# Performance work log

Hardware: AMD Instinct MI355X
Metric: run time of the kernel (lower is better)

Reference implementation:

```python
import jax, jax.numpy as jnp
import numpy as np

B, S, D, H = 2, 2048, 1024, 16
DH = D // H
DFF = 4 * D
EPS = 1e-5
NEG = -1e9


def _layernorm(x, gamma, beta):
    mu = jnp.mean(x, axis=-1, keepdims=True)
    var = jnp.mean(jnp.square(x - mu), axis=-1, keepdims=True)
    return (x - mu) * jax.lax.rsqrt(var + EPS) * gamma + beta


def setup_inputs() -> dict:
    key = jax.random.key(0)
    ks = jax.random.split(key, 12)
    s = 0.02
    X = jax.random.normal(ks[0], (B, S, D), dtype=jnp.float32)
    # causal mask (True = attend)
    attention_mask = jnp.tril(jnp.ones((S, S), dtype=bool))
    return {
        "X": X,
        "attention_mask": attention_mask,
        "gamma1": jnp.ones((D,), jnp.float32),
        "beta1": jnp.zeros((D,), jnp.float32),
        "Wq": jax.random.normal(ks[1], (H, D, DH), jnp.float32) * s,
        "bq": jnp.zeros((H, DH), jnp.float32),
        "Wk": jax.random.normal(ks[2], (H, D, DH), jnp.float32) * s,
        "bk": jnp.zeros((H, DH), jnp.float32),
        "Wv": jax.random.normal(ks[3], (H, D, DH), jnp.float32) * s,
        "bv": jnp.zeros((H, DH), jnp.float32),
        "W0": jax.random.normal(ks[4], (D, D), jnp.float32) * s,
        "b0": jnp.zeros((D,), jnp.float32),
        "gamma2": jnp.ones((D,), jnp.float32),
        "beta2": jnp.zeros((D,), jnp.float32),
        "W1": jax.random.normal(ks[5], (D, DFF), jnp.float32) * s,
        "b1": jnp.zeros((DFF,), jnp.float32),
        "W2": jax.random.normal(ks[6], (DFF, D), jnp.float32) * s,
        "b2": jnp.zeros((D,), jnp.float32),
    }


def reference(X, attention_mask, gamma1, beta1, Wq, bq, Wk, bk, Wv, bv, W0, b0,
              gamma2, beta2, W1, b1, W2, b2):
    scale = 1.0 / np.sqrt(DH)
    # --- pre-LN MHA ---
    Xn = _layernorm(X, gamma1, beta1)
    # per-head projections, stacked: [B,H,S,DH]
    Q = jnp.einsum('bsd,hdk->bhsk', Xn, Wq) + bq[None, :, None, :]
    K = jnp.einsum('bsd,hdk->bhsk', Xn, Wk) + bk[None, :, None, :]
    V = jnp.einsum('bsd,hdk->bhsk', Xn, Wv) + bv[None, :, None, :]
    scores = jnp.einsum('bhsk,bhtk->bhst', Q, K) * scale
    scores = jnp.where(attention_mask, scores, NEG)
    weights = jax.nn.softmax(scores, axis=-1)
    attn = jnp.einsum('bhst,bhtv->bhsv', weights, V)  # [B,H,S,DH]
    # concat heads (head-major along feature dim, matching torch.cat order)
    attn = attn.transpose(0, 2, 1, 3).reshape(B, S, D)
    mha = attn @ W0 + b0
    X = mha + X  # residual (dropout = identity at eval)
    # --- pre-LN FFN ---
    Xn2 = _layernorm(X, gamma2, beta2)
    h = jax.nn.relu(Xn2 @ W1 + b1)
    ffn = h @ W2 + b2
    return ffn + X
```

## Files before the change

kernel.cpp:

```cpp
#include <hip/hip_runtime.h>
#include <hip/hip_bf16.h>

#define BB 2
#define SS 2048
#define DDIM 1024
#define HH 16
#define DHH 64
#define DFF_ 4096
#define BS 4096
#define NQKV 3072

typedef unsigned short u16;
using short8  = __attribute__((ext_vector_type(8))) short;
using floatx4 = __attribute__((ext_vector_type(4))) float;

__device__ __forceinline__ u16 f2b(float f){
  union { unsigned int u; float f; } v; v.f = f;
  unsigned int u = v.u;
  u += 0x7FFFu + ((u >> 16) & 1u);
  return (u16)(u >> 16);
}

__device__ __forceinline__ void gl2lds16(const u16* g, u16* l){
  __builtin_amdgcn_global_load_lds((const __attribute__((address_space(1))) void*)g,
                                   (__attribute__((address_space(3))) void*)l, 16, 0, 0);
}

__device__ __forceinline__ void ln_row(const float* __restrict__ x,
                                       const float* __restrict__ gamma,
                                       const float* __restrict__ beta,
                                       u16* __restrict__ y, int row, float* smem){
  const float4* xr = (const float4*)(x + (size_t)row * DDIM);
  int tid = threadIdx.x;
  float4 v = xr[tid];
  float s  = v.x + v.y + v.z + v.w;
  float ss = v.x*v.x + v.y*v.y + v.z*v.z + v.w*v.w;
  for (int o = 1; o < 64; o <<= 1){ s += __shfl_xor(s, o, 64); ss += __shfl_xor(ss, o, 64); }
  int wid = tid >> 6;
  if ((tid & 63) == 0){ smem[wid] = s; smem[wid + 4] = ss; }
  __syncthreads();
  s  = smem[0] + smem[1] + smem[2] + smem[3];
  ss = smem[4] + smem[5] + smem[6] + smem[7];
  float mu  = s / (float)DDIM;
  float var = ss / (float)DDIM - mu * mu;
  float rs  = rsqrtf(var + 1e-5f);
  const float4* gp = (const float4*)gamma;
  const float4* bp = (const float4*)beta;
  float4 g = gp[tid], b = bp[tid];
  u16* yr = y + (size_t)row * DDIM + tid*4;
  yr[0] = f2b((v.x - mu) * rs * g.x + b.x);
  yr[1] = f2b((v.y - mu) * rs * g.y + b.y);
  yr[2] = f2b((v.z - mu) * rs * g.z + b.z);
  yr[3] = f2b((v.w - mu) * rs * g.w + b.w);
}

__device__ __forceinline__ void tcast(const float* __restrict__ in, u16* __restrict__ out,
                                      int R, int C, int tile, float (*sh)[33]){
  int nr = R >> 5;
  int tr = tile % nr, tc = tile / nr;
  int r0 = tr * 32, c0 = tc * 32;
  int tx = threadIdx.x & 31, ty = threadIdx.x >> 5;
  for (int i = ty; i < 32; i += 8)
    sh[i][tx] = in[(size_t)(r0 + i) * C + c0 + tx];
  __syncthreads();
  for (int i = ty; i < 32; i += 8)
    out[(size_t)(c0 + i) * R + r0 + tx] = f2b(sh[tx][i]);
}

__global__ __launch_bounds__(256) void prep_ln1_k(
    const float* __restrict__ X, const float* __restrict__ g1, const float* __restrict__ be1,
    u16* __restrict__ Xn,
    const float* __restrict__ Wq, const float* __restrict__ Wk, const float* __restrict__ Wv,
    const float* __restrict__ W0, const float* __restrict__ W1,
    const float* __restrict__ bq, const float* __restrict__ bk, const float* __restrict__ bv,
    u16* __restrict__ wqkvT, u16* __restrict__ w0T, u16* __restrict__ w1T,
    float* __restrict__ biasQKV)
{
  __shared__ float sh[32][33];
  __shared__ float smem8[8];
  int id = blockIdx.x;
  if (id < 4096){
    ln_row(X, g1, be1, Xn, id, smem8);
  } else if (id < 7168){
    int lid2 = id - 4096;
    int which = lid2 >> 10, lid = lid2 & 1023;
    const float* src = which == 0 ? Wq : (which == 1 ? Wk : Wv);
    u16* dst = wqkvT + (size_t)which * 1048576;
    int bat = lid >> 6, t = lid & 63;
    tcast(src + (size_t)bat * 65536, dst + (size_t)bat * 65536, 1024, 64, t, sh);
  } else if (id < 8192){
    tcast(W0, w0T, 1024, 1024, id - 7168, sh);
  } else if (id < 12288){
    tcast(W1, w1T, 1024, 4096, id - 8192, sh);
  } else {
    int idx = (id - 12288) * 256 + threadIdx.x;
    if (idx < 3072){
      float v = idx < 1024 ? bq[idx] : (idx < 2048 ? bk[idx - 1024] : bv[idx - 2048]);
      biasQKV[idx] = v;
    }
  }
}

__global__ __launch_bounds__(256) void w2t_ln2_k(
    const float* __restrict__ X1, const float* __restrict__ g2, const float* __restrict__ be2,
    u16* __restrict__ Xn2, const float* __restrict__ W2, u16* __restrict__ w2T)
{
  __shared__ float sh[32][33];
  __shared__ float smem8[8];
  int id = blockIdx.x;
  if (id < 4096){
    ln_row(X1, g2, be2, Xn2, id, smem8);
  } else {
    int tile = id - 4096;
    int tr = tile / 32, tc = tile % 32;
    int r0 = tr * 32, c0 = tc * 32;
    int tx = threadIdx.x & 31, ty = threadIdx.x >> 5;
    for (int i = ty; i < 32; i += 8)
      sh[i][tx] = W2[(size_t)(r0 + i) * 1024 + c0 + tx];
    __syncthreads();
    for (int i = ty; i < 32; i += 8)
      w2T[(size_t)(c0 + i) * 4096 + r0 + tx] = f2b(sh[tx][i]);
  }
}

__global__ __launch_bounds__(256) void vt_k(const u16* __restrict__ QKV, u16* __restrict__ VT){
  __shared__ u16 t[32][33];
  int bh = blockIdx.z; int b = bh >> 4, h = bh & 15;
  int s0 = blockIdx.x * 32, d0 = blockIdx.y * 32;
  int tx = threadIdx.x & 31, ty = threadIdx.x >> 5;
  const u16* src = QKV + (size_t)b * SS * NQKV + 2048 + h * DHH;
  for (int i = ty; i < 32; i += 8)
    t[i][tx] = src[(size_t)(s0 + i) * NQKV + d0 + tx];
  __syncthreads();
  u16* dst = VT + (size_t)bh * DHH * SS;
  for (int i = ty; i < 32; i += 8)
    dst[(size_t)(d0 + i) * SS + s0 + tx] = t[tx][i];
}

template<int TM, int TN>
__global__ __launch_bounds__(256) void gemm_k(
    const u16* __restrict__ A, const u16* __restrict__ Bt,
    const float* __restrict__ bias, const float* __restrict__ res,
    void* __restrict__ Cv, int M, int N, int K, int relu, int writeBf16)
{
  constexpr int ACH = TM / 16;
  constexpr int BCH = TN / 16;
  constexpr int CH1 = ACH + BCH;
  constexpr int CPW = (2 * CH1) / 4;
  constexpr int MI  = TM / 32;
  constexpr int NI  = TN / 32;

  __shared__ __align__(16) u16 As[2][TM * 32];
  __shared__ __align__(16) u16 Bs[2][TN * 32];

  int tid  = threadIdx.x;
  int wave = tid >> 6, lane = tid & 63;
  int quad = lane >> 4, l16 = lane & 15;

  int gx = gridDim.x, gy = gridDim.y;
  int bid = blockIdx.x + gx * blockIdx.y;
  int xcd = bid & 7, idx = bid >> 3;
  int by  = xcd * (gy >> 3) + idx / gx;
  int bx  = idx % gx;

  int m0 = by * TM, n0 = bx * TN;
  int wm = (wave >> 1) * (TM / 2), wn = (wave & 1) * (TN / 2);

  floatx4 acc[MI][NI] = {};

  int srow = lane >> 2;
  int scol = (lane & 3) * 8;
  const u16* gptr[CPW]; u16* lptr[CPW];
#pragma unroll
  for (int k = 0; k < CPW; k++){
    int c = wave * CPW + k;
    int p = c / CH1, cc = c % CH1;
    if (cc < ACH){
      gptr[k] = A  + (size_t)(m0 + cc*16 + srow) * K + p*32 + scol;
      lptr[k] = &As[p][cc * 512];
    } else {
      gptr[k] = Bt + (size_t)(n0 + (cc-ACH)*16 + srow) * K + p*32 + scol;
      lptr[k] = &Bs[p][(cc-ACH) * 512];
    }
  }

  for (int kt = 0; kt < K; kt += 64){
#pragma unroll
    for (int k = 0; k < CPW; k++){ gl2lds16(gptr[k], lptr[k]); gptr[k] += 64; }
    __syncthreads();
#pragma unroll
    for (int p = 0; p < 2; p++){
      short8 af[MI], bf[NI];
#pragma unroll
      for (int i = 0; i < MI; i++)
        af[i] = *(short8*)&As[p][(wm + i*16 + l16)*32 + quad*8];
#pragma unroll
      for (int j = 0; j < NI; j++)
        bf[j] = *(short8*)&Bs[p][(wn + j*16 + l16)*32 + quad*8];
#pragma unroll
      for (int i = 0; i < MI; i++)
#pragma unroll
        for (int j = 0; j < NI; j++)
          acc[i][j] = __builtin_amdgcn_mfma_f32_16x16x32_bf16(af[i], bf[j], acc[i][j], 0,0,0);
    }
    __syncthreads();
  }

  u16*   Cb = (u16*)Cv;
  float* Cf = (float*)Cv;
#pragma unroll
  for (int j = 0; j < NI; j++){
    int col = n0 + wn + j*16 + l16;
    float bj = bias ? bias[col] : 0.f;
#pragma unroll
    for (int i = 0; i < MI; i++){
#pragma unroll
      for (int r = 0; r < 4; r++){
        int row = m0 + wm + i*16 + quad*4 + r;
        float v = acc[i][j][r] + bj;
        if (relu) v = v > 0.f ? v : 0.f;
        if (res)  v += res[(size_t)row * N + col];
        if (writeBf16) Cb[(size_t)row * N + col] = f2b(v);
        else           Cf[(size_t)row * N + col] = v;
      }
    }
  }
}

#define KT   128
#define KsLD 72
#define VTLD 136
#define PsLD 136

__global__ __launch_bounds__(256) void attn_k(
    const u16* __restrict__ QKV, const u16* __restrict__ VT, u16* __restrict__ O)
{
  int bh = blockIdx.x;
  int b = bh >> 4, h = bh & 15;
  int qt = (int)gridDim.y - 1 - blockIdx.y;
  int q0 = qt * 64;
  const u16* Qb_  = QKV + (size_t)b * SS * NQKV + h * DHH;
  const u16* Kb_  = Qb_ + 1024;
  const u16* VTb_ = VT + (size_t)bh * DHH * SS;

  __shared__ __align__(16) u16 Ks [KT * KsLD];
  __shared__ __align__(16) u16 VTs[DHH * VTLD];
  __shared__ __align__(16) u16 Ps [4][16 * PsLD];

  int tid = threadIdx.x;
  int wave = tid >> 6, lane = tid & 63;
  int quad = lane >> 4, l16 = lane & 15;
  int qrow = q0 + wave * 16;

  short8 qf0, qf1;
  {
    const u16* qp = Qb_ + (size_t)(qrow + l16) * NQKV + quad*8;
    qf0 = *(const short8*)qp;
    qf1 = *(const short8*)(qp + 32);
  }

  float l_acc[4] = {0.f, 0.f, 0.f, 0.f};
  floatx4 oacc[4] = {};

  int nk = (qt >> 1) + 1;
  int lim = wave + 4 * (qt & 1);
  const float qs = 0.125f * 1.44269504088896f;

  for (int kt = 0; kt < nk; kt++){
    int k0 = kt * KT;
    __syncthreads();
#pragma unroll
    for (int it = 0; it < 4; it++){
      int g = tid + it * 256;
      {
        int row = g >> 3, c = (g & 7) * 8;
        *(short8*)&Ks[row * KsLD + c] = *(const short8*)(Kb_ + (size_t)(k0 + row) * NQKV + c);
      }
      {
        int dh = g >> 4, c = (g & 15) * 8;
        *(short8*)&VTs[dh * VTLD + c] = *(const short8*)(VTb_ + (size_t)dh * SS + k0 + c);
      }
    }
    __syncthreads();

    bool last = (kt == nk - 1);
    int stmax = last ? lim : 7;
    floatx4 sacc[8] = {};
#pragma unroll
    for (int st = 0; st < 8; st++){
      if (st <= stmax){
        short8 kb0 = *(short8*)&Ks[(st*16 + l16) * KsLD + quad*8];
        short8 kb1 = *(short8*)&Ks[(st*16 + l16) * KsLD + 32 + quad*8];
        sacc[st] = __builtin_amdgcn_mfma_f32_16x16x32_bf16(qf0, kb0, sacc[st], 0,0,0);
        sacc[st] = __builtin_amdgcn_mfma_f32_16x16x32_bf16(qf1, kb1, sacc[st], 0,0,0);
      }
    }

#pragma unroll
    for (int st = 0; st < 8; st++){
      if (st <= stmax){
        if (last){
          int col = k0 + st*16 + l16;
#pragma unroll
          for (int r = 0; r < 4; r++){
            float e = exp2f(sacc[st][r] * qs);
            e = (col <= qrow + quad*4 + r) ? e : 0.f;
            l_acc[r] += e;
            Ps[wave][(quad*4 + r) * PsLD + st*16 + l16] = f2b(e);
          }
        } else {
#pragma unroll
          for (int r = 0; r < 4; r++){
            float e = exp2f(sacc[st][r] * qs);
            l_acc[r] += e;
            Ps[wave][(quad*4 + r) * PsLD + st*16 + l16] = f2b(e);
          }
        }
      } else {
#pragma unroll
        for (int r = 0; r < 4; r++)
          Ps[wave][(quad*4 + r) * PsLD + st*16 + l16] = 0;
      }
    }
    asm volatile("s_waitcnt lgkmcnt(0)" ::: "memory");

    int cmax = last ? (lim >> 1) : 3;
    short8 pa[4];
#pragma unroll
    for (int c = 0; c < 4; c++)
      pa[c] = *(short8*)&Ps[wave][l16 * PsLD + c*32 + quad*8];
#pragma unroll
    for (int ost = 0; ost < 4; ost++){
#pragma unroll
      for (int c = 0; c < 4; c++){
        if (c <= cmax){
          short8 vb = *(short8*)&VTs[(ost*16 + l16) * VTLD + c*32 + quad*8];
          oacc[ost] = __builtin_amdgcn_mfma_f32_16x16x32_bf16(pa[c], vb, oacc[ost], 0,0,0);
        }
      }
    }
  }

#pragma unroll
  for (int r = 0; r < 4; r++){
    for (int o = 1; o < 16; o <<= 1) l_acc[r] += __shfl_xor(l_acc[r], o, 64);
  }
  float inv[4];
#pragma unroll
  for (int r = 0; r < 4; r++) inv[r] = 1.0f / l_acc[r];

#pragma unroll
  for (int ost = 0; ost < 4; ost++)
#pragma unroll
    for (int r = 0; r < 4; r++){
      int s  = qrow + quad*4 + r;
      int dh = ost*16 + l16;
      O[((size_t)b * SS + s) * DDIM + h * DHH + dh] = f2b(oacc[ost][r] * inv[r]);
    }
}

extern "C" void kernel_launch(void* const* d_in, const int* in_sizes, int n_in,
                              void* d_out, int out_size, void* d_ws, size_t ws_size,
                              hipStream_t stream) {
  const float* X   = (const float*)d_in[0];
  const float* g1  = (const float*)d_in[2];
  const float* be1 = (const float*)d_in[3];
  const float* Wq  = (const float*)d_in[4];
  const float* bq  = (const float*)d_in[5];
  const float* Wk  = (const float*)d_in[6];
  const float* bk  = (const float*)d_in[7];
  const float* Wv  = (const float*)d_in[8];
  const float* bv  = (const float*)d_in[9];
  const float* W0  = (const float*)d_in[10];
  const float* b0  = (const float*)d_in[11];
  const float* g2  = (const float*)d_in[12];
  const float* be2 = (const float*)d_in[13];
  const float* W1  = (const float*)d_in[14];
  const float* b1  = (const float*)d_in[15];
  const float* W2  = (const float*)d_in[16];
  const float* b2  = (const float*)d_in[17];
  float* out = (float*)d_out;

  u16* ws16 = (u16*)d_ws;
  u16* wqkvT = ws16;
  u16* w0T   = ws16 + 3145728;
  u16* w2T   = ws16;
  u16* w1T   = ws16 + 4194304;
  u16* QKVb  = ws16 + 8388608;
  u16* VTb   = ws16 + 8388608 + 12582912;
  u16* hb    = ws16 + 8388608;
  u16* Xn    = ws16 + 25165824;
  u16* attnB = Xn;
  float* biasQKV = (float*)(ws16 + 29360128);

  prep_ln1_k<<<dim3(12300), 256, 0, stream>>>(X, g1, be1, Xn,
      Wq, Wk, Wv, W0, W1, bq, bk, bv, wqkvT, w0T, w1T, biasQKV);

  gemm_k<128,128><<<dim3(24, 32), 256, 0, stream>>>(Xn, wqkvT, biasQKV, nullptr, QKVb,
      BS, NQKV, 1024, 0, 1);

  vt_k<<<dim3(64, 2, 32), 256, 0, stream>>>(QKVb, VTb);

  attn_k<<<dim3(32, 32), 256, 0, stream>>>(QKVb, VTb, attnB);

  gemm_k<64,128><<<dim3(8, 64), 256, 0, stream>>>(attnB, w0T, b0, X, out,
      BS, DDIM, 1024, 0, 0);

  w2t_ln2_k<<<dim3(8192), 256, 0, stream>>>(out, g2, be2, Xn, W2, w2T);

  gemm_k<128,128><<<dim3(32, 32), 256, 0, stream>>>(Xn, w1T, b1, nullptr, hb,
      BS, DFF_, 1024, 1, 1);
  gemm_k<64,128><<<dim3(8, 64), 256, 0, stream>>>(hb, w2T, b2, out, out,
      BS, DDIM, DFF_, 0, 0);
}
```

Baseline: 423.4 us.

## Split-K the two N=1024 GEMMs with atomic accumulation into pre-seeded output

The W0 and W2 projection GEMMs, which launch only 512 blocks, now split K across gridDim.z (2 and 4 slices) and accumulate partial sums into the fp32 output with atomicAdd. The residual X is copied into the output during the LN1 pass so the atomic adds build on it, and only slice 0 adds the bias. This raises block count and occupancy on the many-CU device. The cost is atomic traffic, an extra write of X, and non-deterministic summation order.

```diff
diff --git a/kernel.cpp b/kernel.cpp
--- a/kernel.cpp
+++ b/kernel.cpp
@@ -29,10 +29,12 @@
 __device__ __forceinline__ void ln_row(const float* __restrict__ x,
                                        const float* __restrict__ gamma,
                                        const float* __restrict__ beta,
-                                       u16* __restrict__ y, int row, float* smem){
+                                       u16* __restrict__ y, int row, float* smem,
+                                       float* __restrict__ xcopy){
   const float4* xr = (const float4*)(x + (size_t)row * DDIM);
   int tid = threadIdx.x;
   float4 v = xr[tid];
+  if (xcopy) ((float4*)(xcopy + (size_t)row * DDIM))[tid] = v;
   float s  = v.x + v.y + v.z + v.w;
   float ss = v.x*v.x + v.y*v.y + v.z*v.z + v.w*v.w;
   for (int o = 1; o < 64; o <<= 1){ s += __shfl_xor(s, o, 64); ss += __shfl_xor(ss, o, 64); }
@@ -74,13 +76,13 @@
     const float* __restrict__ W0, const float* __restrict__ W1,
     const float* __restrict__ bq, const float* __restrict__ bk, const float* __restrict__ bv,
     u16* __restrict__ wqkvT, u16* __restrict__ w0T, u16* __restrict__ w1T,
-    float* __restrict__ biasQKV)
+    float* __restrict__ biasQKV, float* __restrict__ Xout)
 {
   __shared__ float sh[32][33];
   __shared__ float smem8[8];
   int id = blockIdx.x;
   if (id < 4096){
-    ln_row(X, g1, be1, Xn, id, smem8);
+    ln_row(X, g1, be1, Xn, id, smem8, Xout);
   } else if (id < 7168){
     int lid2 = id - 4096;
     int which = lid2 >> 10, lid = lid2 & 1023;
@@ -109,7 +111,7 @@
   __shared__ float smem8[8];
   int id = blockIdx.x;
   if (id < 4096){
-    ln_row(X1, g2, be2, Xn2, id, smem8);
+    ln_row(X1, g2, be2, Xn2, id, smem8, nullptr);
   } else {
     int tile = id - 4096;
     int tr = tile / 32, tc = tile % 32;
@@ -141,7 +143,7 @@
 __global__ __launch_bounds__(256) void gemm_k(
     const u16* __restrict__ A, const u16* __restrict__ Bt,
     const float* __restrict__ bias, const float* __restrict__ res,
-    void* __restrict__ Cv, int M, int N, int K, int relu, int writeBf16)
+    void* __restrict__ Cv, int M, int N, int K, int relu, int writeBf16, int atomicOut)
 {
   constexpr int ACH = TM / 16;
   constexpr int BCH = TN / 16;
@@ -163,6 +165,10 @@
   int by  = xcd * (gy >> 3) + idx / gx;
   int bx  = idx % gx;
 
+  int kz = blockIdx.z;
+  int Kc = K / (int)gridDim.z;
+  int kbase = kz * Kc;
+
   int m0 = by * TM, n0 = bx * TN;
   int wm = (wave >> 1) * (TM / 2), wn = (wave & 1) * (TN / 2);
 
@@ -176,15 +182,15 @@
     int c = wave * CPW + k;
     int p = c / CH1, cc = c % CH1;
     if (cc < ACH){
-      gptr[k] = A  + (size_t)(m0 + cc*16 + srow) * K + p*32 + scol;
+      gptr[k] = A  + (size_t)(m0 + cc*16 + srow) * K + kbase + p*32 + scol;
       lptr[k] = &As[p][cc * 512];
     } else {
-      gptr[k] = Bt + (size_t)(n0 + (cc-ACH)*16 + srow) * K + p*32 + scol;
+      gptr[k] = Bt + (size_t)(n0 + (cc-ACH)*16 + srow) * K + kbase + p*32 + scol;
       lptr[k] = &Bs[p][(cc-ACH) * 512];
     }
   }
 
-  for (int kt = 0; kt < K; kt += 64){
+  for (int kt = 0; kt < Kc; kt += 64){
 #pragma unroll
     for (int k = 0; k < CPW; k++){ gl2lds16(gptr[k], lptr[k]); gptr[k] += 64; }
     __syncthreads();
@@ -211,7 +217,7 @@
 #pragma unroll
   for (int j = 0; j < NI; j++){
     int col = n0 + wn + j*16 + l16;
-    float bj = bias ? bias[col] : 0.f;
+    float bj = (bias && (!atomicOut || kz == 0)) ? bias[col] : 0.f;
 #pragma unroll
     for (int i = 0; i < MI; i++){
 #pragma unroll
@@ -219,9 +225,13 @@
         int row = m0 + wm + i*16 + quad*4 + r;
         float v = acc[i][j][r] + bj;
         if (relu) v = v > 0.f ? v : 0.f;
-        if (res)  v += res[(size_t)row * N + col];
-        if (writeBf16) Cb[(size_t)row * N + col] = f2b(v);
-        else           Cf[(size_t)row * N + col] = v;
+        if (atomicOut){
+          atomicAdd(&Cf[(size_t)row * N + col], v);
+        } else {
+          if (res)  v += res[(size_t)row * N + col];
+          if (writeBf16) Cb[(size_t)row * N + col] = f2b(v);
+          else           Cf[(size_t)row * N + col] = v;
+        }
       }
     }
   }
@@ -394,22 +404,23 @@
   float* biasQKV = (float*)(ws16 + 29360128);
 
   prep_ln1_k<<<dim3(12300), 256, 0, stream>>>(X, g1, be1, Xn,
-      Wq, Wk, Wv, W0, W1, bq, bk, bv, wqkvT, w0T, w1T, biasQKV);
+      Wq, Wk, Wv, W0, W1, bq, bk, bv, wqkvT, w0T, w1T, biasQKV, out);
 
   gemm_k<128,128><<<dim3(24, 32), 256, 0, stream>>>(Xn, wqkvT, biasQKV, nullptr, QKVb,
-      BS, NQKV, 1024, 0, 1);
+      BS, NQKV, 1024, 0, 1, 0);
 
   vt_k<<<dim3(64, 2, 32), 256, 0, stream>>>(QKVb, VTb);
 
   attn_k<<<dim3(32, 32), 256, 0, stream>>>(QKVb, VTb, attnB);
 
-  gemm_k<64,128><<<dim3(8, 64), 256, 0, stream>>>(attnB, w0T, b0, X, out,
-      BS, DDIM, 1024, 0, 0);
+  gemm_k<64,128><<<dim3(8, 64, 2), 256, 0, stream>>>(attnB, w0T, b0, nullptr, out,
+      BS, DDIM, 1024, 0, 0, 1);
 
   w2t_ln2_k<<<dim3(8192), 256, 0, stream>>>(out, g2, be2, Xn, W2, w2T);
 
   gemm_k<128,128><<<dim3(32, 32), 256, 0, stream>>>(Xn, w1T, b1, nullptr, hb,
-      BS, DFF_, 1024, 1, 1);
-  gemm_k<64,128><<<dim3(8, 64), 256, 0, stream>>>(hb, w2T, b2, out, out,
-      BS, DDIM, DFF_, 0, 0);
-}
+      BS, DFF_, 1024, 1, 1, 0);
+
+  gemm_k<64,128><<<dim3(8, 64, 4), 256, 0, stream>>>(hb, w2T, b2, nullptr, out,
+      BS, DDIM, DFF_, 0, 0, 1);
+}
```

New measurement: 441.8 us. 1.04x slower.
